# Optimization experiments

Hardware: AMD Instinct MI355X
Metric: run time of the kernel (lower is better)

## Reference

```python
import jax, jax.numpy as jnp
import numpy as np

FEAT_DIM = 1024
NUM_HEAD = 8


def setup_inputs() -> dict:
    key = jax.random.key(0)
    ks = jax.random.split(key, 8)
    D = FEAT_DIM
    s = D ** -0.5
    return {
        "motion": jax.random.normal(ks[0], (8, 1024, D), dtype=jnp.float32),
        "scene_feats": jax.random.normal(ks[1], (8, 2048, D), dtype=jnp.float32),
        # nn.Linear weights stored as [in, out] (already transposed for x @ W)
        "Wq": jax.random.normal(ks[2], (D, D), dtype=jnp.float32) * s,
        "bq": jax.random.normal(ks[3], (D,), dtype=jnp.float32) * s,
        "Wkv": jax.random.normal(ks[4], (D, 2 * D), dtype=jnp.float32) * s,
        "bkv": jax.random.normal(ks[5], (2 * D,), dtype=jnp.float32) * s,
        "Wout": jax.random.normal(ks[6], (D, D), dtype=jnp.float32) * s,
        "bout": jax.random.normal(ks[7], (D,), dtype=jnp.float32) * s,
    }


def reference(motion, scene_feats, Wq, bq, Wkv, bkv, Wout, bout):
    bs, L, D = motion.shape
    N = scene_feats.shape[1]
    H = NUM_HEAD
    Dh = D // H

    # q scaled by full feat_dim**-0.5 (as in source, not head_dim)
    q = (motion @ Wq + bq) * (D ** -0.5)
    kv = scene_feats @ Wkv + bkv
    k, v = kv[..., :D], kv[..., D:]

    # Faithful to source: q is viewed as (bs, H, L, Dh) with NO transpose,
    # while k, v use view(bs, N, H, Dh) followed by transpose(1, 2).
    q = q.reshape(bs, H, L, Dh)                      # [bs,H,L,Dh] (layout quirk)
    k = k.reshape(bs, N, H, Dh).transpose(0, 2, 1, 3)  # [bs,H,N,Dh]
    v = v.reshape(bs, N, H, Dh).transpose(0, 2, 1, 3)  # [bs,H,N,Dh]

    att = jnp.einsum("bhld,bhnd->bhln", q, k)        # [bs,H,L,N]
    att = jax.nn.softmax(att, axis=-1)
    out = jnp.einsum("bhln,bhnd->bhld", att, v)      # [bs,H,L,Dh]
    out = out.reshape(bs, L, D)                      # contiguous view, matches torch .view
    return out @ Wout + bout
```

## Files before the change

kernel.cpp:

```cpp
#include <hip/hip_runtime.h>

typedef __attribute__((ext_vector_type(8))) short bf16x8;
typedef __attribute__((ext_vector_type(4))) float f32x4;
typedef __attribute__((ext_vector_type(4))) float f32x4v;

#define MFMA16(a,b,c) __builtin_amdgcn_mfma_f32_16x16x32_bf16((a),(b),(c),0,0,0)

__device__ __forceinline__ short f2bf(float f){
  unsigned u = __builtin_bit_cast(unsigned, f);
  u += 0x7fffu + ((u >> 16) & 1u);
  return (short)(u >> 16);
}

__device__ __forceinline__ void gload16(const void* g, void* l){
  __builtin_amdgcn_global_load_lds((const __attribute__((address_space(1))) unsigned*)g,
                                   (__attribute__((address_space(3))) unsigned*)l,
                                   16, 0, 0);
}

__global__ __launch_bounds__(256) void k_f2bf(const float* __restrict__ in,
                                              short* __restrict__ out, int n8){
  int i = blockIdx.x * 256 + threadIdx.x;
  if (i >= n8) return;
  f32x4v a = ((const f32x4v*)in)[i*2];
  f32x4v b = ((const f32x4v*)in)[i*2+1];
  bf16x8 o;
  o[0]=f2bf(a[0]); o[1]=f2bf(a[1]); o[2]=f2bf(a[2]); o[3]=f2bf(a[3]);
  o[4]=f2bf(b[0]); o[5]=f2bf(b[1]); o[6]=f2bf(b[2]); o[7]=f2bf(b[3]);
  ((bf16x8*)out)[i] = o;
}

__global__ __launch_bounds__(256) void k_prep_wT(const float* __restrict__ W,
                                                 short* __restrict__ Wt, int K, int N){
  int i = blockIdx.x * 256 + threadIdx.x;
  int total = (K >> 3) * N;
  if (i >= total) return;
  int n  = i % N;
  int k0 = (i / N) << 3;
  bf16x8 o;
#pragma unroll
  for (int j = 0; j < 8; ++j) o[j] = f2bf(W[(size_t)(k0 + j) * N + n]);
  *(bf16x8*)&Wt[(size_t)n * K + k0] = o;
}

template<int MODE>
__global__ __launch_bounds__(256, 4) void k_gemm(
    const short* __restrict__ A, const short* __restrict__ Bt,
    const float* __restrict__ bias, float scale,
    void* __restrict__ out0, void* __restrict__ out1,
    int M, int N, int K)
{
  __shared__ __align__(16) short Alds[3][128 * 32];
  __shared__ __align__(16) short Blds[3][128 * 32];
  const int tid = threadIdx.x;
  const int l = tid & 63, w = tid >> 6;
  const int wr = w >> 1, wc = w & 1;
  const int lr = l & 15, lg = l >> 4;

  const int nx = gridDim.x;
  const int nwg = nx * gridDim.y;
  int flat = blockIdx.y * nx + blockIdx.x;
  int u = (flat & 7) * (nwg >> 3) + (flat >> 3);
  const int m0 = (u / nx) * 128, n0 = (u % nx) * 128;

  const int srow = l >> 2;
  const int scol = 8 * ((l & 3) ^ ((l >> 3) & 3));
  const int acol = 8 * (lg ^ ((lr >> 1) & 3));

  f32x4 acc[4][4];
#pragma unroll
  for (int a = 0; a < 4; ++a)
#pragma unroll
    for (int b = 0; b < 4; ++b) acc[a][b] = (f32x4)(0.0f);

  const int nk = K >> 5;
  auto stage = [&](int kt, int slot){
    int k0 = kt << 5;
#pragma unroll
    for (int i = 0; i < 4; ++i){
      int c = w * 4 + i;
      if (c < 8){
        int m = c * 16 + srow;
        gload16(A + (size_t)(m0 + m) * K + k0 + scol, &Alds[slot][c * 512]);
      } else {
        int n = (c - 8) * 16 + srow;
        gload16(Bt + (size_t)(n0 + n) * K + k0 + scol, &Blds[slot][(c - 8) * 512]);
      }
    }
  };

  stage(0, 0);
  stage(1, 1);
  int rd = 0;
  for (int kt = 0; kt < nk; ++kt){
    asm volatile("s_waitcnt vmcnt(4)" ::: "memory");
    __builtin_amdgcn_s_barrier();
    __builtin_amdgcn_sched_barrier(0);
    int tt = (kt + 2 < nk) ? kt + 2 : nk - 1;
    int tgt = rd + 2; if (tgt >= 3) tgt -= 3;
    stage(tt, tgt);

    bf16x8 af[4], bfv[4];
#pragma unroll
    for (int mi = 0; mi < 4; ++mi){
      int row = wr * 64 + mi * 16 + lr;
      af[mi] = *(const bf16x8*)&Alds[rd][row * 32 + acol];
    }
#pragma unroll
    for (int ni = 0; ni < 4; ++ni){
      int row = wc * 64 + ni * 16 + lr;
      bfv[ni] = *(const bf16x8*)&Blds[rd][row * 32 + acol];
    }
#pragma unroll
    for (int mi = 0; mi < 4; ++mi)
#pragma unroll
      for (int ni = 0; ni < 4; ++ni)
        acc[mi][ni] = MFMA16(af[mi], bfv[ni], acc[mi][ni]);

    if (++rd == 3) rd = 0;
  }
  asm volatile("s_waitcnt vmcnt(0)" ::: "memory");

#pragma unroll
  for (int mi = 0; mi < 4; ++mi)
#pragma unroll
    for (int ni = 0; ni < 4; ++ni){
      int col = n0 + wc * 64 + ni * 16 + lr;
      float bv = bias[col];
#pragma unroll
      for (int r = 0; r < 4; ++r){
        int row = m0 + wr * 64 + mi * 16 + lg * 4 + r;
        float v = acc[mi][ni][r] + bv;
        if (MODE == 0){
          v *= scale;
          int b = row >> 10, lp = row & 1023;
          int h = lp >> 7;
          int lq = ((lp & 127) << 3) | (col >> 7);
          int dh = col & 127;
          ((short*)out0)[(((size_t)(b * 8 + h)) * 1024 + lq) * 128 + dh] = f2bf(v);
        } else {
          ((float*)out0)[(size_t)row * N + col] = v;
        }
      }
    }
}

__global__ __launch_bounds__(512, 2) void k_gemmKV(
    const short* __restrict__ A, const short* __restrict__ Bt,
    const float* __restrict__ bias,
    short* __restrict__ out0, short* __restrict__ out1)
{
  __shared__ __align__(16) short As[3][256 * 32];
  __shared__ __align__(16) short Bs[3][256 * 32];
  const int tid = threadIdx.x;
  const int l = tid & 63, w = tid >> 6;
  const int lr = l & 15, lg = l >> 4;
  const int wm = w >> 2, wn = w & 3;

  int flat = blockIdx.y * 8 + blockIdx.x;
  int u = (flat & 7) * 64 + (flat >> 3);
  const int m0 = (u >> 3) * 256, n0 = (u & 7) * 256;

  const int srow = l >> 2;
  const int scol = 8 * ((l & 3) ^ ((l >> 3) & 3));
  const int acol = 8 * (lg ^ ((lr >> 1) & 3));

  f32x4 acc[8][4];
#pragma unroll
  for (int a = 0; a < 8; ++a)
#pragma unroll
    for (int b = 0; b < 4; ++b) acc[a][b] = (f32x4)(0.0f);

  auto stage = [&](int kt, int slot){
    int k0 = kt << 5;
#pragma unroll
    for (int i = 0; i < 4; ++i){
      int c = w * 4 + i;
      if (c < 16){
        int m = c * 16 + srow;
        gload16(A + (size_t)(m0 + m) * 1024 + k0 + scol, &As[slot][c * 512]);
      } else {
        int n = (c - 16) * 16 + srow;
        gload16(Bt + (size_t)(n0 + n) * 1024 + k0 + scol, &Bs[slot][(c - 16) * 512]);
      }
    }
  };

  stage(0, 0);
  stage(1, 1);
  int rd = 0;
  for (int kt = 0; kt < 32; ++kt){
    asm volatile("s_waitcnt vmcnt(4)" ::: "memory");
    __builtin_amdgcn_s_barrier();
    __builtin_amdgcn_sched_barrier(0);
    int tt = (kt + 2 < 32) ? kt + 2 : 31;
    int tgt = rd + 2; if (tgt >= 3) tgt -= 3;
    stage(tt, tgt);

    bf16x8 af[8], bfv[4];
#pragma unroll
    for (int mi = 0; mi < 8; ++mi){
      int row = wm * 128 + mi * 16 + lr;
      af[mi] = *(const bf16x8*)&As[rd][row * 32 + acol];
    }
#pragma unroll
    for (int ni = 0; ni < 4; ++ni){
      int row = wn * 64 + ni * 16 + lr;
      bfv[ni] = *(const bf16x8*)&Bs[rd][row * 32 + acol];
    }
    __builtin_amdgcn_s_setprio(1);
#pragma unroll
    for (int mi = 0; mi < 8; ++mi)
#pragma unroll
      for (int ni = 0; ni < 4; ++ni)
        acc[mi][ni] = MFMA16(af[mi], bfv[ni], acc[mi][ni]);
    __builtin_amdgcn_s_setprio(0);

    if (++rd == 3) rd = 0;
  }
  asm volatile("s_waitcnt vmcnt(0)" ::: "memory");

#pragma unroll
  for (int mi = 0; mi < 8; ++mi)
#pragma unroll
    for (int ni = 0; ni < 4; ++ni){
      int col = n0 + wn * 64 + ni * 16 + lr;
      float bv = bias[col];
#pragma unroll
      for (int r = 0; r < 4; ++r){
        int row = m0 + wm * 128 + mi * 16 + lg * 4 + r;
        float v = acc[mi][ni][r] + bv;
        int b = row >> 11, nn = row & 2047;
        if (col < 1024){
          int h = col >> 7, dh = col & 127;
          out0[(((size_t)(b * 8 + h)) * 2048 + nn) * 128 + dh] = f2bf(v);
        } else {
          int c2 = col - 1024, h = c2 >> 7, dh = c2 & 127;
          out1[(((size_t)(b * 8 + h)) * 128 + dh) * 2048 + nn] = f2bf(v);
        }
      }
    }
}

__global__ __launch_bounds__(512, 2) void k_attn(
    const short* __restrict__ Q, const short* __restrict__ K,
    const short* __restrict__ Vt, short* __restrict__ O)
{
  __shared__ __align__(16) short Klds[2][64 * 128];
  __shared__ __align__(16) short Vlds[2][128 * 64];
  __shared__ __align__(16) short Plds[8][32 * 64];
  const int tid = threadIdx.x;
  const int l = tid & 63, w = tid >> 6;
  const int lr = l & 15, lg = l >> 4;

  int flat = blockIdx.y * 4 + blockIdx.x;
  int xcd = flat & 7, idx = flat >> 3;
  int bh = xcd * 8 + (idx >> 2);
  int q0 = (idx & 3) * 256;

  const short* Qb = Q  + (size_t)bh * 1024 * 128;
  const short* Kb = K  + (size_t)bh * 2048 * 128;
  const short* Vb = Vt + (size_t)bh * 128 * 2048;

  bf16x8 qf[2][4];
#pragma unroll
  for (int mi = 0; mi < 2; ++mi)
#pragma unroll
    for (int kc = 0; kc < 4; ++kc)
      qf[mi][kc] = *(const bf16x8*)&Qb[(size_t)(q0 + w * 32 + mi * 16 + lr) * 128 + kc * 32 + lg * 8];

  f32x4 acc[8][2];
#pragma unroll
  for (int d = 0; d < 8; ++d){ acc[d][0] = (f32x4)(0.0f); acc[d][1] = (f32x4)(0.0f); }
  float mrun[2][4], lsum[2][4];
#pragma unroll
  for (int mi = 0; mi < 2; ++mi)
#pragma unroll
    for (int r = 0; r < 4; ++r){ mrun[mi][r] = -3e38f; lsum[mi][r] = 0.f; }

  auto stageK = [&](int t, int buf){
    int kv0 = t * 64;
#pragma unroll
    for (int i = 0; i < 2; ++i){
      int c = w * 2 + i;
      int row = 4 * c + (l >> 4);
      int col = ((l & 15) * 8) ^ ((row & 7) * 8);
      gload16(Kb + (size_t)(kv0 + row) * 128 + col, &Klds[buf][c * 512]);
    }
  };
  auto stageV = [&](int t, int buf){
    int kv0 = t * 64;
#pragma unroll
    for (int i = 0; i < 2; ++i){
      int c = w * 2 + i;
      int dh = 8 * c + (l >> 3);
      int col = ((l & 7) * 8) ^ (((l >> 3) & 7) * 8);
      gload16(Vb + (size_t)dh * 2048 + kv0 + col, &Vlds[buf][c * 512]);
    }
  };

  stageK(0, 0); stageV(0, 0);
  __syncthreads();
  int cur = 0;
  const int swz = (lr & 7) * 8;

  for (int t = 0; t < 32; ++t){
    if (t + 1 < 32){ stageK(t + 1, cur ^ 1); stageV(t + 1, cur ^ 1); }
    const short* Kl = &Klds[cur][0];
    const short* Vl = &Vlds[cur][0];
    short* Pw = &Plds[w][0];

    f32x4 s[2][4];
    __builtin_amdgcn_s_setprio(1);
#pragma unroll
    for (int nt = 0; nt < 4; ++nt){
      f32x4 s0 = (f32x4)(0.0f), s1 = (f32x4)(0.0f);
#pragma unroll
      for (int kc = 0; kc < 4; ++kc){
        bf16x8 kf = *(const bf16x8*)&Kl[(nt * 16 + lr) * 128 + ((kc * 32 + lg * 8) ^ swz)];
        s0 = MFMA16(qf[0][kc], kf, s0);
        s1 = MFMA16(qf[1][kc], kf, s1);
      }
      s[0][nt] = s0; s[1][nt] = s1;
    }
    __builtin_amdgcn_s_setprio(0);

    float pmax[2][4];
    int ok = 1;
#pragma unroll
    for (int mi = 0; mi < 2; ++mi)
#pragma unroll
      for (int r = 0; r < 4; ++r){
        float v = fmaxf(fmaxf(s[mi][0][r], s[mi][1][r]), fmaxf(s[mi][2][r], s[mi][3][r]));
        pmax[mi][r] = v;
        ok &= (v <= mrun[mi][r] + 8.0f) ? 1 : 0;
      }
    if (!__all(ok)){
#pragma unroll
      for (int mi = 0; mi < 2; ++mi)
#pragma unroll
        for (int r = 0; r < 4; ++r){
          float v = pmax[mi][r];
          v = fmaxf(v, __shfl_xor(v, 1, 16));
          v = fmaxf(v, __shfl_xor(v, 2, 16));
          v = fmaxf(v, __shfl_xor(v, 4, 16));
          v = fmaxf(v, __shfl_xor(v, 8, 16));
          float mnew = fmaxf(mrun[mi][r], v);
          float sc = exp2f(mrun[mi][r] - mnew);
          mrun[mi][r] = mnew;
          lsum[mi][r] *= sc;
#pragma unroll
          for (int d = 0; d < 8; ++d) acc[d][mi][r] *= sc;
        }
    }

#pragma unroll
    for (int mi = 0; mi < 2; ++mi)
#pragma unroll
      for (int r = 0; r < 4; ++r){
        int row = mi * 16 + lg * 4 + r;
        int rsw = (row & 7) * 8;
        float ls = 0.f;
#pragma unroll
        for (int nt = 0; nt < 4; ++nt){
          float p = exp2f(s[mi][nt][r] - mrun[mi][r]);
          ls += p;
          Pw[row * 64 + ((nt * 16 + lr) ^ rsw)] = f2bf(p);
        }
        lsum[mi][r] += ls;
      }

    bf16x8 pa[2][2];
#pragma unroll
    for (int mi = 0; mi < 2; ++mi)
#pragma unroll
      for (int kc = 0; kc < 2; ++kc)
        pa[mi][kc] = *(const bf16x8*)&Pw[(mi * 16 + lr) * 64 + ((kc * 32 + lg * 8) ^ swz)];
    __builtin_amdgcn_s_setprio(1);
#pragma unroll
    for (int d = 0; d < 8; ++d)
#pragma unroll
      for (int kc = 0; kc < 2; ++kc){
        bf16x8 vf = *(const bf16x8*)&Vl[(d * 16 + lr) * 64 + ((kc * 32 + lg * 8) ^ swz)];
        acc[d][0] = MFMA16(pa[0][kc], vf, acc[d][0]);
        acc[d][1] = MFMA16(pa[1][kc], vf, acc[d][1]);
      }
    __builtin_amdgcn_s_setprio(0);

    __syncthreads();
    cur ^= 1;
  }

  const int b = bh >> 3, h = bh & 7;
#pragma unroll
  for (int mi = 0; mi < 2; ++mi)
#pragma unroll
    for (int r = 0; r < 4; ++r){
      float ls = lsum[mi][r];
      ls += __shfl_xor(ls, 1, 16);
      ls += __shfl_xor(ls, 2, 16);
      ls += __shfl_xor(ls, 4, 16);
      ls += __shfl_xor(ls, 8, 16);
      float inv = 1.0f / ls;
      int grow = q0 + w * 32 + mi * 16 + lg * 4 + r;
      size_t base = ((size_t)b * 1024 + (size_t)h * 128 + (grow >> 3)) * 1024
                  + (size_t)(grow & 7) * 128;
#pragma unroll
      for (int d = 0; d < 8; ++d)
        O[base + d * 16 + lr] = f2bf(acc[d][mi][r] * inv);
    }
}

extern "C" void kernel_launch(void* const* d_in, const int* in_sizes, int n_in,
                              void* d_out, int out_size, void* d_ws, size_t ws_size,
                              hipStream_t stream){
  const float* motion = (const float*)d_in[0];
  const float* scene  = (const float*)d_in[1];
  const float* Wq     = (const float*)d_in[2];
  const float* bq     = (const float*)d_in[3];
  const float* Wkv    = (const float*)d_in[4];
  const float* bkv    = (const float*)d_in[5];
  const float* Wout   = (const float*)d_in[6];
  const float* bout   = (const float*)d_in[7];
  float* out = (float*)d_out;

  char* ws = (char*)d_ws;
  const size_t MB = 1024 * 1024;
  short* WqT   = (short*)(ws + 0);
  short* WkvT  = (short*)(ws + 2  * MB);
  short* WoutT = (short*)(ws + 6  * MB);
  short* mA    = (short*)(ws + 8  * MB);
  short* sA    = (short*)(ws + 24 * MB);
  short* Qb    = (short*)(ws + 56 * MB);
  short* Kb    = (short*)(ws + 72 * MB);
  short* Vtb   = (short*)(ws + 104* MB);
  short* attnO = mA;

  const float qscale = 0.03125f * 1.44269504088896341f;

  k_prep_wT<<<dim3(512),  256, 0, stream>>>(Wq,   WqT,   1024, 1024);
  k_prep_wT<<<dim3(1024), 256, 0, stream>>>(Wkv,  WkvT,  1024, 2048);
  k_prep_wT<<<dim3(512),  256, 0, stream>>>(Wout, WoutT, 1024, 1024);
  k_f2bf<<<dim3(4096), 256, 0, stream>>>(motion, mA, 1024 * 1024);
  k_f2bf<<<dim3(8192), 256, 0, stream>>>(scene,  sA, 2 * 1024 * 1024);

  k_gemm<0><<<dim3(8, 64), 256, 0, stream>>>(mA, WqT, bq, qscale, Qb, nullptr, 8192, 1024, 1024);
  k_gemmKV<<<dim3(8, 64), 512, 0, stream>>>(sA, WkvT, bkv, Kb, Vtb);
  k_attn<<<dim3(4, 64), 512, 0, stream>>>(Qb, Kb, Vtb, attnO);
  k_gemm<2><<<dim3(8, 64), 256, 0, stream>>>(attnO, WoutT, bout, 1.0f, out, nullptr, 8192, 1024, 1024);
}
```

Baseline: 303.6 us.

## Keep softmax probabilities in registers via transposed S and bpermute; halve attention blocks

Result: no change. 302.9 us (-0.3%).

```diff
diff --git a/kernel.cpp b/kernel.cpp
--- a/kernel.cpp
+++ b/kernel.cpp
@@ -3,6 +3,7 @@
 typedef __attribute__((ext_vector_type(8))) short bf16x8;
 typedef __attribute__((ext_vector_type(4))) float f32x4;
 typedef __attribute__((ext_vector_type(4))) float f32x4v;
+typedef __attribute__((ext_vector_type(4))) int i32x4;
 
 #define MFMA16(a,b,c) __builtin_amdgcn_mfma_f32_16x16x32_bf16((a),(b),(c),0,0,0)
 
@@ -16,6 +17,12 @@
   __builtin_amdgcn_global_load_lds((const __attribute__((address_space(1))) unsigned*)g,
                                    (__attribute__((address_space(3))) unsigned*)l,
                                    16, 0, 0);
+}
+
+__device__ __forceinline__ int packbf(float a, float b){
+  unsigned ua = __builtin_bit_cast(unsigned, a) + 0x7fffu;
+  unsigned ub = __builtin_bit_cast(unsigned, b) + 0x7fffu;
+  return __builtin_amdgcn_perm(ub, ua, 0x07060302);
 }
 
 __global__ __launch_bounds__(256) void k_f2bf(const float* __restrict__ in,
@@ -242,21 +249,21 @@
     }
 }
 
-__global__ __launch_bounds__(512, 2) void k_attn(
+__global__ __launch_bounds__(256, 2) void k_attn(
     const short* __restrict__ Q, const short* __restrict__ K,
     const short* __restrict__ Vt, short* __restrict__ O)
 {
   __shared__ __align__(16) short Klds[2][64 * 128];
   __shared__ __align__(16) short Vlds[2][128 * 64];
-  __shared__ __align__(16) short Plds[8][32 * 64];
   const int tid = threadIdx.x;
   const int l = tid & 63, w = tid >> 6;
   const int lr = l & 15, lg = l >> 4;
 
-  int flat = blockIdx.y * 4 + blockIdx.x;
+  int flat = blockIdx.y * 8 + blockIdx.x;
   int xcd = flat & 7, idx = flat >> 3;
-  int bh = xcd * 8 + (idx >> 2);
-  int q0 = (idx & 3) * 256;
+  int bh = xcd * 8 + (idx >> 3);
+  int q0 = (idx & 7) * 128;
+  const int qbase = q0 + w * 32;
 
   const short* Qb = Q  + (size_t)bh * 1024 * 128;
   const short* Kb = K  + (size_t)bh * 2048 * 128;
@@ -267,22 +274,24 @@
   for (int mi = 0; mi < 2; ++mi)
 #pragma unroll
     for (int kc = 0; kc < 4; ++kc)
-      qf[mi][kc] = *(const bf16x8*)&Qb[(size_t)(q0 + w * 32 + mi * 16 + lr) * 128 + kc * 32 + lg * 8];
-
-  f32x4 acc[8][2];
-#pragma unroll
-  for (int d = 0; d < 8; ++d){ acc[d][0] = (f32x4)(0.0f); acc[d][1] = (f32x4)(0.0f); }
-  float mrun[2][4], lsum[2][4];
+      qf[mi][kc] = *(const bf16x8*)&Qb[(size_t)(qbase + mi * 16 + lr) * 128 + kc * 32 + lg * 8];
+
+  f32x4 acc[2][8];
 #pragma unroll
   for (int mi = 0; mi < 2; ++mi)
 #pragma unroll
-    for (int r = 0; r < 4; ++r){ mrun[mi][r] = -3e38f; lsum[mi][r] = 0.f; }
+    for (int d = 0; d < 8; ++d) acc[mi][d] = (f32x4)(0.0f);
+  float mrun[2] = {-3e38f, -3e38f}, lsum[2] = {0.f, 0.f};
+
+  const int addrA = 4 * ((l & 15) + 32 * ((l >> 4) & 1));
+  const int addrB = addrA + 64;
+  const bool hi = (l >= 32);
 
   auto stageK = [&](int t, int buf){
     int kv0 = t * 64;
 #pragma unroll
-    for (int i = 0; i < 2; ++i){
-      int c = w * 2 + i;
+    for (int i = 0; i < 4; ++i){
+      int c = w * 4 + i;
       int row = 4 * c + (l >> 4);
       int col = ((l & 15) * 8) ^ ((row & 7) * 8);
       gload16(Kb + (size_t)(kv0 + row) * 128 + col, &Klds[buf][c * 512]);
@@ -291,8 +300,8 @@
   auto stageV = [&](int t, int buf){
     int kv0 = t * 64;
 #pragma unroll
-    for (int i = 0; i < 2; ++i){
-      int c = w * 2 + i;
+    for (int i = 0; i < 4; ++i){
+      int c = w * 4 + i;
       int dh = 8 * c + (l >> 3);
       int col = ((l & 7) * 8) ^ (((l >> 3) & 7) * 8);
       gload16(Vb + (size_t)dh * 2048 + kv0 + col, &Vlds[buf][c * 512]);
@@ -308,7 +317,6 @@
     if (t + 1 < 32){ stageK(t + 1, cur ^ 1); stageV(t + 1, cur ^ 1); }
     const short* Kl = &Klds[cur][0];
     const short* Vl = &Vlds[cur][0];
-    short* Pw = &Plds[w][0];
 
     f32x4 s[2][4];
     __builtin_amdgcn_s_setprio(1);
@@ -318,72 +326,87 @@
 #pragma unroll
       for (int kc = 0; kc < 4; ++kc){
         bf16x8 kf = *(const bf16x8*)&Kl[(nt * 16 + lr) * 128 + ((kc * 32 + lg * 8) ^ swz)];
-        s0 = MFMA16(qf[0][kc], kf, s0);
-        s1 = MFMA16(qf[1][kc], kf, s1);
+        s0 = MFMA16(kf, qf[0][kc], s0);
+        s1 = MFMA16(kf, qf[1][kc], s1);
       }
       s[0][nt] = s0; s[1][nt] = s1;
     }
     __builtin_amdgcn_s_setprio(0);
 
-    float pmax[2][4];
+    float mloc[2];
     int ok = 1;
 #pragma unroll
+    for (int mi = 0; mi < 2; ++mi){
+      float v = fmaxf(fmaxf(fmaxf(s[mi][0][0], s[mi][0][1]), fmaxf(s[mi][0][2], s[mi][0][3])),
+                      fmaxf(fmaxf(s[mi][1][0], s[mi][1][1]), fmaxf(s[mi][1][2], s[mi][1][3])));
+      v = fmaxf(v, fmaxf(fmaxf(fmaxf(s[mi][2][0], s[mi][2][1]), fmaxf(s[mi][2][2], s[mi][2][3])),
+                         fmaxf(fmaxf(s[mi][3][0], s[mi][3][1]), fmaxf(s[mi][3][2], s[mi][3][3]))));
+      mloc[mi] = v;
+      ok &= (v <= mrun[mi] + 8.0f) ? 1 : 0;
+    }
+    if (!__all(ok)){
+#pragma unroll
+      for (int mi = 0; mi < 2; ++mi){
+        float v = mloc[mi];
+        v = fmaxf(v, __shfl_xor(v, 16));
+        v = fmaxf(v, __shfl_xor(v, 32));
+        float mnew = fmaxf(mrun[mi], v);
+        float sc = exp2f(mrun[mi] - mnew);
+        mrun[mi] = mnew;
+        lsum[mi] *= sc;
+#pragma unroll
+        for (int r = 0; r < 4; ++r){
+          float scr = __shfl(sc, 20 * lg + r);
+#pragma unroll
+          for (int d = 0; d < 8; ++d) acc[mi][d][r] *= scr;
+        }
+      }
+    }
+
+    int pk[2][4][2];
+#pragma unroll
+    for (int mi = 0; mi < 2; ++mi){
+      float ls = 0.f;
+#pragma unroll
+      for (int nt = 0; nt < 4; ++nt){
+        float p0 = exp2f(s[mi][nt][0] - mrun[mi]);
+        float p1 = exp2f(s[mi][nt][1] - mrun[mi]);
+        float p2 = exp2f(s[mi][nt][2] - mrun[mi]);
+        float p3 = exp2f(s[mi][nt][3] - mrun[mi]);
+        ls += (p0 + p1) + (p2 + p3);
+        pk[mi][nt][0] = packbf(p0, p1);
+        pk[mi][nt][1] = packbf(p2, p3);
+      }
+      lsum[mi] += ls;
+    }
+
+    bf16x8 pa[2][2];
+#pragma unroll
     for (int mi = 0; mi < 2; ++mi)
 #pragma unroll
-      for (int r = 0; r < 4; ++r){
-        float v = fmaxf(fmaxf(s[mi][0][r], s[mi][1][r]), fmaxf(s[mi][2][r], s[mi][3][r]));
-        pmax[mi][r] = v;
-        ok &= (v <= mrun[mi][r] + 8.0f) ? 1 : 0;
-      }
-    if (!__all(ok)){
-#pragma unroll
-      for (int mi = 0; mi < 2; ++mi)
-#pragma unroll
-        for (int r = 0; r < 4; ++r){
-          float v = pmax[mi][r];
-          v = fmaxf(v, __shfl_xor(v, 1, 16));
-          v = fmaxf(v, __shfl_xor(v, 2, 16));
-          v = fmaxf(v, __shfl_xor(v, 4, 16));
-          v = fmaxf(v, __shfl_xor(v, 8, 16));
-          float mnew = fmaxf(mrun[mi][r], v);
-          float sc = exp2f(mrun[mi][r] - mnew);
-          mrun[mi][r] = mnew;
-          lsum[mi][r] *= sc;
-#pragma unroll
-          for (int d = 0; d < 8; ++d) acc[d][mi][r] *= sc;
+      for (int kc = 0; kc < 2; ++kc){
+        i32x4 dw;
+#pragma unroll
+        for (int av = 0; av < 2; ++av){
+          int addr = av ? addrB : addrA;
+#pragma unroll
+          for (int jj = 0; jj < 2; ++jj){
+            int t0 = __builtin_amdgcn_ds_bpermute(addr, pk[mi][2 * kc][jj]);
+            int t1 = __builtin_amdgcn_ds_bpermute(addr, pk[mi][2 * kc + 1][jj]);
+            dw[av * 2 + jj] = hi ? t1 : t0;
+          }
         }
-    }
-
-#pragma unroll
-    for (int mi = 0; mi < 2; ++mi)
-#pragma unroll
-      for (int r = 0; r < 4; ++r){
-        int row = mi * 16 + lg * 4 + r;
-        int rsw = (row & 7) * 8;
-        float ls = 0.f;
-#pragma unroll
-        for (int nt = 0; nt < 4; ++nt){
-          float p = exp2f(s[mi][nt][r] - mrun[mi][r]);
-          ls += p;
-          Pw[row * 64 + ((nt * 16 + lr) ^ rsw)] = f2bf(p);
-        }
-        lsum[mi][r] += ls;
-      }
-
-    bf16x8 pa[2][2];
-#pragma unroll
-    for (int mi = 0; mi < 2; ++mi)
-#pragma unroll
-      for (int kc = 0; kc < 2; ++kc)
-        pa[mi][kc] = *(const bf16x8*)&Pw[(mi * 16 + lr) * 64 + ((kc * 32 + lg * 8) ^ swz)];
+        pa[mi][kc] = __builtin_bit_cast(bf16x8, dw);
+      }
+
     __builtin_amdgcn_s_setprio(1);
 #pragma unroll
     for (int d = 0; d < 8; ++d)
 #pragma unroll
       for (int kc = 0; kc < 2; ++kc){
         bf16x8 vf = *(const bf16x8*)&Vl[(d * 16 + lr) * 64 + ((kc * 32 + lg * 8) ^ swz)];
-        acc[d][0] = MFMA16(pa[0][kc], vf, acc[d][0]);
-        acc[d][1] = MFMA16(pa[1][kc], vf, acc[d][1]);
+        acc[0][d] = MFMA16(pa[0][kc], vf, acc[0][d]);
+        acc[1][d] = MFMA16(pa[1][kc], vf, acc[1][d]);
       }
     __builtin_amdgcn_s_setprio(0);
 
@@ -393,22 +416,22 @@
 
   const int b = bh >> 3, h = bh & 7;
 #pragma unroll
-  for (int mi = 0; mi < 2; ++mi)
+  for (int mi = 0; mi < 2; ++mi){
+    float ls = lsum[mi];
+    ls += __shfl_xor(ls, 16);
+    ls += __shfl_xor(ls, 32);
+    float inv = 1.0f / ls;
 #pragma unroll
     for (int r = 0; r < 4; ++r){
-      float ls = lsum[mi][r];
-      ls += __shfl_xor(ls, 1, 16);
-      ls += __shfl_xor(ls, 2, 16);
-      ls += __shfl_xor(ls, 4, 16);
-      ls += __shfl_xor(ls, 8, 16);
-      float inv = 1.0f / ls;
-      int grow = q0 + w * 32 + mi * 16 + lg * 4 + r;
+      float invr = __shfl(inv, 20 * lg + r);
+      int grow = qbase + mi * 16 + lg * 4 + r;
       size_t base = ((size_t)b * 1024 + (size_t)h * 128 + (grow >> 3)) * 1024
                   + (size_t)(grow & 7) * 128;
 #pragma unroll
       for (int d = 0; d < 8; ++d)
-        O[base + d * 16 + lr] = f2bf(acc[d][mi][r] * inv);
-    }
+        O[base + d * 16 + lr] = f2bf(acc[mi][d][r] * invr);
+    }
+  }
 }
 
 extern "C" void kernel_launch(void* const* d_in, const int* in_sizes, int n_in,
@@ -446,6 +469,6 @@
 
   k_gemm<0><<<dim3(8, 64), 256, 0, stream>>>(mA, WqT, bq, qscale, Qb, nullptr, 8192, 1024, 1024);
   k_gemmKV<<<dim3(8, 64), 512, 0, stream>>>(sA, WkvT, bkv, Kb, Vtb);
-  k_attn<<<dim3(4, 64), 512, 0, stream>>>(Qb, Kb, Vtb, attnO);
+  k_attn<<<dim3(8, 64), 256, 0, stream>>>(Qb, Kb, Vtb, attnO);
   k_gemm<2><<<dim3(8, 64), 256, 0, stream>>>(attnO, WoutT, bout, 1.0f, out, nullptr, 8192, 1024, 1024);
 }
```

## Restructure attention to compute S transposed and pass P via register permutes

Applied to the files above, without the earlier changes.

Result: slower. 324.3 us (+6.8%).

```diff
diff --git a/kernel.cpp b/kernel.cpp
--- a/kernel.cpp
+++ b/kernel.cpp
@@ -3,6 +3,7 @@
 typedef __attribute__((ext_vector_type(8))) short bf16x8;
 typedef __attribute__((ext_vector_type(4))) float f32x4;
 typedef __attribute__((ext_vector_type(4))) float f32x4v;
+typedef __attribute__((ext_vector_type(4))) int i32x4;
 
 #define MFMA16(a,b,c) __builtin_amdgcn_mfma_f32_16x16x32_bf16((a),(b),(c),0,0,0)
 
@@ -16,6 +17,12 @@
   __builtin_amdgcn_global_load_lds((const __attribute__((address_space(1))) unsigned*)g,
                                    (__attribute__((address_space(3))) unsigned*)l,
                                    16, 0, 0);
+}
+
+__device__ __forceinline__ int packbf(float a, float b){
+  unsigned ua = __builtin_bit_cast(unsigned, a) + 0x7fffu;
+  unsigned ub = __builtin_bit_cast(unsigned, b) + 0x7fffu;
+  return __builtin_amdgcn_perm(ub, ua, 0x07060302);
 }
 
 __global__ __launch_bounds__(256) void k_f2bf(const float* __restrict__ in,
@@ -158,8 +165,7 @@
   const int wm = w >> 2, wn = w & 3;
 
   int flat = blockIdx.y * 8 + blockIdx.x;
-  int u = (flat & 7) * 64 + (flat >> 3);
-  const int m0 = (u >> 3) * 256, n0 = (u & 7) * 256;
+  const int m0 = (flat >> 3) * 256, n0 = (flat & 7) * 256;
 
   const int srow = l >> 2;
   const int scol = 8 * ((l & 3) ^ ((l >> 3) & 3));
@@ -242,44 +248,38 @@
     }
 }
 
-__global__ __launch_bounds__(512, 2) void k_attn(
+__global__ __launch_bounds__(256, 4) void k_attn(
     const short* __restrict__ Q, const short* __restrict__ K,
     const short* __restrict__ Vt, short* __restrict__ O)
 {
-  __shared__ __align__(16) short Klds[2][64 * 128];
-  __shared__ __align__(16) short Vlds[2][128 * 64];
-  __shared__ __align__(16) short Plds[8][32 * 64];
+  __shared__ __align__(16) short Klds[2][32 * 128];
+  __shared__ __align__(16) short Vlds[2][128 * 32];
   const int tid = threadIdx.x;
   const int l = tid & 63, w = tid >> 6;
   const int lr = l & 15, lg = l >> 4;
 
-  int flat = blockIdx.y * 4 + blockIdx.x;
+  int flat = blockIdx.y * 8 + blockIdx.x;
   int xcd = flat & 7, idx = flat >> 3;
-  int bh = xcd * 8 + (idx >> 2);
-  int q0 = (idx & 3) * 256;
+  int bh = xcd * 8 + (idx >> 4);
+  int q0 = (idx & 15) * 64;
+  const int qbase = q0 + w * 16;
 
   const short* Qb = Q  + (size_t)bh * 1024 * 128;
   const short* Kb = K  + (size_t)bh * 2048 * 128;
   const short* Vb = Vt + (size_t)bh * 128 * 2048;
 
-  bf16x8 qf[2][4];
-#pragma unroll
-  for (int mi = 0; mi < 2; ++mi)
-#pragma unroll
-    for (int kc = 0; kc < 4; ++kc)
-      qf[mi][kc] = *(const bf16x8*)&Qb[(size_t)(q0 + w * 32 + mi * 16 + lr) * 128 + kc * 32 + lg * 8];
-
-  f32x4 acc[8][2];
-#pragma unroll
-  for (int d = 0; d < 8; ++d){ acc[d][0] = (f32x4)(0.0f); acc[d][1] = (f32x4)(0.0f); }
-  float mrun[2][4], lsum[2][4];
-#pragma unroll
-  for (int mi = 0; mi < 2; ++mi)
-#pragma unroll
-    for (int r = 0; r < 4; ++r){ mrun[mi][r] = -3e38f; lsum[mi][r] = 0.f; }
+  bf16x8 qf[4];
+#pragma unroll
+  for (int kc = 0; kc < 4; ++kc)
+    qf[kc] = *(const bf16x8*)&Qb[(size_t)(qbase + lr) * 128 + kc * 32 + lg * 8];
+
+  f32x4 acc[8];
+#pragma unroll
+  for (int d = 0; d < 8; ++d) acc[d] = (f32x4)(0.0f);
+  float mrun = -3e38f, lsum = 0.f;
 
   auto stageK = [&](int t, int buf){
-    int kv0 = t * 64;
+    int kv0 = t * 32;
 #pragma unroll
     for (int i = 0; i < 2; ++i){
       int c = w * 2 + i;
@@ -289,12 +289,12 @@
     }
   };
   auto stageV = [&](int t, int buf){
-    int kv0 = t * 64;
+    int kv0 = t * 32;
 #pragma unroll
     for (int i = 0; i < 2; ++i){
       int c = w * 2 + i;
-      int dh = 8 * c + (l >> 3);
-      int col = ((l & 7) * 8) ^ (((l >> 3) & 7) * 8);
+      int dh = c * 16 + (l >> 2);
+      int col = ((l & 3) * 8) ^ (((l >> 2) & 3) * 8);
       gload16(Vb + (size_t)dh * 2048 + kv0 + col, &Vlds[buf][c * 512]);
     }
   };
@@ -302,89 +302,73 @@
   stageK(0, 0); stageV(0, 0);
   __syncthreads();
   int cur = 0;
-  const int swz = (lr & 7) * 8;
-
-  for (int t = 0; t < 32; ++t){
-    if (t + 1 < 32){ stageK(t + 1, cur ^ 1); stageV(t + 1, cur ^ 1); }
+  const int kswz = (lr & 7) * 8;
+  const int vswz = (lr & 3) * 8;
+
+  for (int t = 0; t < 64; ++t){
+    if (t + 1 < 64){ stageK(t + 1, cur ^ 1); stageV(t + 1, cur ^ 1); }
     const short* Kl = &Klds[cur][0];
     const short* Vl = &Vlds[cur][0];
-    short* Pw = &Plds[w][0];
-
-    f32x4 s[2][4];
+
+    f32x4 s[2];
     __builtin_amdgcn_s_setprio(1);
 #pragma unroll
-    for (int nt = 0; nt < 4; ++nt){
-      f32x4 s0 = (f32x4)(0.0f), s1 = (f32x4)(0.0f);
+    for (int nt = 0; nt < 2; ++nt){
+      f32x4 sv = (f32x4)(0.0f);
 #pragma unroll
       for (int kc = 0; kc < 4; ++kc){
-        bf16x8 kf = *(const bf16x8*)&Kl[(nt * 16 + lr) * 128 + ((kc * 32 + lg * 8) ^ swz)];
-        s0 = MFMA16(qf[0][kc], kf, s0);
-        s1 = MFMA16(qf[1][kc], kf, s1);
-      }
-      s[0][nt] = s0; s[1][nt] = s1;
+        bf16x8 kf = *(const bf16x8*)&Kl[(nt * 16 + lr) * 128 + ((kc * 32 + lg * 8) ^ kswz)];
+        sv = MFMA16(kf, qf[kc], sv);
+      }
+      s[nt] = sv;
     }
     __builtin_amdgcn_s_setprio(0);
 
-    float pmax[2][4];
-    int ok = 1;
-#pragma unroll
-    for (int mi = 0; mi < 2; ++mi)
+    float mloc = fmaxf(fmaxf(fmaxf(s[0][0], s[0][1]), fmaxf(s[0][2], s[0][3])),
+                       fmaxf(fmaxf(s[1][0], s[1][1]), fmaxf(s[1][2], s[1][3])));
+    if (!__all(mloc <= mrun + 8.0f)){
+      float v = mloc;
+      v = fmaxf(v, __shfl_xor(v, 16));
+      v = fmaxf(v, __shfl_xor(v, 32));
+      float mnew = fmaxf(mrun, v);
+      float sc = exp2f(mrun - mnew);
+      mrun = mnew;
+      lsum *= sc;
 #pragma unroll
       for (int r = 0; r < 4; ++r){
-        float v = fmaxf(fmaxf(s[mi][0][r], s[mi][1][r]), fmaxf(s[mi][2][r], s[mi][3][r]));
-        pmax[mi][r] = v;
-        ok &= (v <= mrun[mi][r] + 8.0f) ? 1 : 0;
-      }
-    if (!__all(ok)){
-#pragma unroll
-      for (int mi = 0; mi < 2; ++mi)
-#pragma unroll
-        for (int r = 0; r < 4; ++r){
-          float v = pmax[mi][r];
-          v = fmaxf(v, __shfl_xor(v, 1, 16));
-          v = fmaxf(v, __shfl_xor(v, 2, 16));
-          v = fmaxf(v, __shfl_xor(v, 4, 16));
-          v = fmaxf(v, __shfl_xor(v, 8, 16));
-          float mnew = fmaxf(mrun[mi][r], v);
-          float sc = exp2f(mrun[mi][r] - mnew);
-          mrun[mi][r] = mnew;
-          lsum[mi][r] *= sc;
-#pragma unroll
-          for (int d = 0; d < 8; ++d) acc[d][mi][r] *= sc;
-        }
-    }
-
-#pragma unroll
-    for (int mi = 0; mi < 2; ++mi)
-#pragma unroll
-      for (int r = 0; r < 4; ++r){
-        int row = mi * 16 + lg * 4 + r;
-        int rsw = (row & 7) * 8;
-        float ls = 0.f;
-#pragma unroll
-        for (int nt = 0; nt < 4; ++nt){
-          float p = exp2f(s[mi][nt][r] - mrun[mi][r]);
-          ls += p;
-          Pw[row * 64 + ((nt * 16 + lr) ^ rsw)] = f2bf(p);
-        }
-        lsum[mi][r] += ls;
-      }
-
-    bf16x8 pa[2][2];
-#pragma unroll
-    for (int mi = 0; mi < 2; ++mi)
-#pragma unroll
-      for (int kc = 0; kc < 2; ++kc)
-        pa[mi][kc] = *(const bf16x8*)&Pw[(mi * 16 + lr) * 64 + ((kc * 32 + lg * 8) ^ swz)];
+        float scr = __shfl(sc, 20 * lg + r);
+#pragma unroll
+        for (int d = 0; d < 8; ++d) acc[d][r] *= scr;
+      }
+    }
+
+    int pk[2][2];
+    {
+      float p0 = exp2f(s[0][0] - mrun), p1 = exp2f(s[0][1] - mrun);
+      float p2 = exp2f(s[0][2] - mrun), p3 = exp2f(s[0][3] - mrun);
+      float p4 = exp2f(s[1][0] - mrun), p5 = exp2f(s[1][1] - mrun);
+      float p6 = exp2f(s[1][2] - mrun), p7 = exp2f(s[1][3] - mrun);
+      lsum += ((p0 + p1) + (p2 + p3)) + ((p4 + p5) + (p6 + p7));
+      pk[0][0] = packbf(p0, p1); pk[0][1] = packbf(p2, p3);
+      pk[1][0] = packbf(p4, p5); pk[1][1] = packbf(p6, p7);
+    }
+
+    i32x4 dw;
+#pragma unroll
+    for (int d4 = 0; d4 < 4; ++d4){
+      int addr = 4 * (lr + 16 * ((2 * lg + (d4 >> 1)) & 3));
+      int t0 = __builtin_amdgcn_ds_bpermute(addr, pk[0][d4 & 1]);
+      int t1 = __builtin_amdgcn_ds_bpermute(addr, pk[1][d4 & 1]);
+      dw[d4] = (lg >= 2) ? t1 : t0;
+    }
+    bf16x8 pa = __builtin_bit_cast(bf16x8, dw);
+
     __builtin_amdgcn_s_setprio(1);
 #pragma unroll
-    for (int d = 0; d < 8; ++d)
-#pragma unroll
-      for (int kc = 0; kc < 2; ++kc){
-        bf16x8 vf = *(const bf16x8*)&Vl[(d * 16 + lr) * 64 + ((kc * 32 + lg * 8) ^ swz)];
-        acc[d][0] = MFMA16(pa[0][kc], vf, acc[d][0]);
-        acc[d][1] = MFMA16(pa[1][kc], vf, acc[d][1]);
-      }
+    for (int d = 0; d < 8; ++d){
+      bf16x8 vf = *(const bf16x8*)&Vl[(d * 16 + lr) * 32 + ((lg * 8) ^ vswz)];
+      acc[d] = MFMA16(pa, vf, acc[d]);
+    }
     __builtin_amdgcn_s_setprio(0);
 
     __syncthreads();
@@ -392,23 +376,20 @@
   }
 
   const int b = bh >> 3, h = bh & 7;
-#pragma unroll
-  for (int mi = 0; mi < 2; ++mi)
-#pragma unroll
-    for (int r = 0; r < 4; ++r){
-      float ls = lsum[mi][r];
-      ls += __shfl_xor(ls, 1, 16);
-      ls += __shfl_xor(ls, 2, 16);
-      ls += __shfl_xor(ls, 4, 16);
-      ls += __shfl_xor(ls, 8, 16);
-      float inv = 1.0f / ls;
-      int grow = q0 + w * 32 + mi * 16 + lg * 4 + r;
-      size_t base = ((size_t)b * 1024 + (size_t)h * 128 + (grow >> 3)) * 1024
-                  + (size_t)(grow & 7) * 128;
-#pragma unroll
-      for (int d = 0; d < 8; ++d)
-        O[base + d * 16 + lr] = f2bf(acc[d][mi][r] * inv);
-    }
+  float ls = lsum;
+  ls += __shfl_xor(ls, 16);
+  ls += __shfl_xor(ls, 32);
+  float inv = 1.0f / ls;
+#pragma unroll
+  for (int r = 0; r < 4; ++r){
+    float invr = __shfl(inv, 20 * lg + r);
+    int grow = qbase + lg * 4 + r;
+    size_t base = ((size_t)b * 1024 + (size_t)h * 128 + (grow >> 3)) * 1024
+                + (size_t)(grow & 7) * 128;
+#pragma unroll
+    for (int d = 0; d < 8; ++d)
+      O[base + d * 16 + lr] = f2bf(acc[d][r] * invr);
+  }
 }
 
 extern "C" void kernel_launch(void* const* d_in, const int* in_sizes, int n_in,
@@ -446,6 +427,6 @@
 
   k_gemm<0><<<dim3(8, 64), 256, 0, stream>>>(mA, WqT, bq, qscale, Qb, nullptr, 8192, 1024, 1024);
   k_gemmKV<<<dim3(8, 64), 512, 0, stream>>>(sA, WkvT, bkv, Kb, Vtb);
-  k_attn<<<dim3(4, 64), 512, 0, stream>>>(Qb, Kb, Vtb, attnO);
+  k_attn<<<dim3(8, 128), 256, 0, stream>>>(Qb, Kb, Vtb, attnO);
   k_gemm<2><<<dim3(8, 64), 256, 0, stream>>>(attnO, WoutT, bout, 1.0f, out, nullptr, 8192, 1024, 1024);
 }
```
